# Optimization experiments

Hardware: AMD Instinct MI355X
Metric: run time of the kernel (lower is better)

## Reference

```python
import jax, jax.numpy as jnp
import numpy as np

LOG2 = float(np.log(2.0))
NEG_INF = float('-inf')


def log1mexp(x):
    # numerically accurate log(1 - exp(x)) for x < 0
    return jnp.where(x > -LOG2, jnp.log(-jnp.expm1(x)), jnp.log1p(-jnp.exp(x)))


def encode_input_log(pos):
    neg = log1mexp(pos)
    # interleave [pos_i, neg_i] then prepend constants [-inf (log 0), 0 (log 1)]
    result = jnp.stack([pos, neg], axis=1).reshape(-1)
    constants = jnp.array([NEG_INF, 0.0], dtype=pos.dtype)
    return jnp.concatenate([constants, result])


def sum_layer(x, ptrs, csr, n):
    # product node in log semiring: segment-sum of gathered log-values
    return jax.ops.segment_sum(x[ptrs], csr, num_segments=n)


def logsum_layer(x, ptrs, csr, n, epsilon=1e-15):
    # sum node in log semiring: numerically stable segment log-sum-exp
    g = x[ptrs]
    m = jax.lax.stop_gradient(jax.ops.segment_max(g, csr, num_segments=n))
    z = g - m[csr]
    z = jnp.nan_to_num(z, nan=0.0, posinf=jnp.inf, neginf=-jnp.inf)  # (-inf)-(-inf) -> 0
    s = jax.ops.segment_sum(jnp.exp(z), csr, num_segments=n) + epsilon
    return jnp.log(s) + m


def setup_inputs() -> dict:
    key = jax.random.key(0)
    n_vars = 2_000_000
    deg = 4
    Ns = [4_000_000, 2_000_000, 1_000_000, 500_000]
    sizes_in = [2 + 2 * n_vars] + Ns[:-1]
    ks = jax.random.split(key, 1 + len(Ns))
    # log-probabilities strictly in (log eps, log(1-eps)) so log1mexp is finite
    u = jax.random.uniform(ks[0], (n_vars,), dtype=jnp.float32, minval=1e-6, maxval=1.0 - 1e-6)
    inp = {"weights": jnp.log(u)}
    for i, n in enumerate(Ns):
        e = n * deg
        inp[f"ptrs{i}"] = jax.random.randint(ks[i + 1], (e,), 0, sizes_in[i], dtype=jnp.int32)
        inp[f"csr{i}"] = jnp.repeat(jnp.arange(n, dtype=jnp.int32), deg)  # unrolled CSR, fan-in=deg
        inp[f"n{i}"] = n
    return inp


def reference(weights, ptrs0, csr0, ptrs1, csr1, ptrs2, csr2, ptrs3, csr3, n0, n1, n2, n3):
    x = encode_input_log(weights)
    x = sum_layer(x, ptrs0, csr0, n0)      # layer 0: product (even)
    x = logsum_layer(x, ptrs1, csr1, n1)   # layer 1: sum (odd)
    x = sum_layer(x, ptrs2, csr2, n2)      # layer 2: product
    x = logsum_layer(x, ptrs3, csr3, n3)   # layer 3: sum
    return x
```

## Files before the change

kernel.cpp:

```cpp
#include <hip/hip_runtime.h>
#include <math.h>

#define NEG_INF (-INFINITY)

typedef int      v4i __attribute__((ext_vector_type(4)));
typedef float    v4f __attribute__((ext_vector_type(4)));
typedef _Float16 v4h __attribute__((ext_vector_type(4)));

__device__ __forceinline__ float fast_log1mexp(float v) {
    if (v > -0.125f) {
        float e = v * (1.0f + v * (0.5f + v * (0.16666667f + v * 0.041666667f)));
        return __logf(-e);
    }
    return __logf(1.0f - __expf(v));
}

__global__ __launch_bounds__(256) void cvt_kernel(const float* __restrict__ w,
                                                  _Float16* __restrict__ wh, int n) {
    int i = blockIdx.x * blockDim.x + threadIdx.x;
    int n4 = n >> 2;
    if (i < n4) {
        v4f v = reinterpret_cast<const v4f*>(w)[i];
        v4h o;
        o.x = (_Float16)v.x; o.y = (_Float16)v.y;
        o.z = (_Float16)v.z; o.w = (_Float16)v.w;
        reinterpret_cast<v4h*>(wh)[i] = o;
    }
    int base = n4 << 2;
    if (i < (n - base)) wh[base + i] = (_Float16)w[base + i];
}

__device__ __forceinline__ float decode_h(const _Float16* __restrict__ wh, int p) {
    int j = (p >> 1) - 1;
    float v = (float)wh[j < 0 ? 0 : j];
    float r = (p & 1) ? fast_log1mexp(v) : v;
    if (p < 2) r = (p == 0) ? NEG_INF : 0.0f;
    return r;
}

__global__ __launch_bounds__(256) void sum4_enc_kernel(const _Float16* __restrict__ wh,
                                                       const v4i* __restrict__ ptrs,
                                                       _Float16* __restrict__ y, int n, int h) {
    int t = blockIdx.x * blockDim.x + threadIdx.x;
    if (t >= h) return;
    v4i pA = __builtin_nontemporal_load(ptrs + t);
    int iB = t + h;
    bool hasB = iB < n;
    v4i pB = hasB ? __builtin_nontemporal_load(ptrs + iB) : pA;
    float a = (decode_h(wh, pA.x) + decode_h(wh, pA.y)) + (decode_h(wh, pA.z) + decode_h(wh, pA.w));
    float b = (decode_h(wh, pB.x) + decode_h(wh, pB.y)) + (decode_h(wh, pB.z) + decode_h(wh, pB.w));
    __builtin_nontemporal_store((_Float16)a, y + t);
    if (hasB) __builtin_nontemporal_store((_Float16)b, y + iB);
}

__global__ __launch_bounds__(256) void sum4_h2h_kernel(const _Float16* __restrict__ x,
                                                       const v4i* __restrict__ ptrs,
                                                       _Float16* __restrict__ y, int n, int h) {
    int t = blockIdx.x * blockDim.x + threadIdx.x;
    if (t >= h) return;
    v4i pA = __builtin_nontemporal_load(ptrs + t);
    int iB = t + h;
    bool hasB = iB < n;
    v4i pB = hasB ? __builtin_nontemporal_load(ptrs + iB) : pA;
    float a = ((float)x[pA.x] + (float)x[pA.y]) + ((float)x[pA.z] + (float)x[pA.w]);
    float b = ((float)x[pB.x] + (float)x[pB.y]) + ((float)x[pB.z] + (float)x[pB.w]);
    __builtin_nontemporal_store((_Float16)a, y + t);
    if (hasB) __builtin_nontemporal_store((_Float16)b, y + iB);
}

__device__ __forceinline__ float lse4(float a, float b, float c, float d) {
    float m = fmaxf(fmaxf(a, b), fmaxf(c, d));
    if (m == NEG_INF) return NEG_INF;
    float s = __expf(a - m) + __expf(b - m) + __expf(c - m) + __expf(d - m) + 1e-15f;
    return __logf(s) + m;
}

__global__ __launch_bounds__(256) void logsum4_h2h_kernel(const _Float16* __restrict__ x,
                                                          const v4i* __restrict__ ptrs,
                                                          _Float16* __restrict__ y, int n, int h) {
    int t = blockIdx.x * blockDim.x + threadIdx.x;
    if (t >= h) return;
    v4i pA = __builtin_nontemporal_load(ptrs + t);
    int iB = t + h;
    bool hasB = iB < n;
    v4i pB = hasB ? __builtin_nontemporal_load(ptrs + iB) : pA;
    float a = lse4((float)x[pA.x], (float)x[pA.y], (float)x[pA.z], (float)x[pA.w]);
    float b = lse4((float)x[pB.x], (float)x[pB.y], (float)x[pB.z], (float)x[pB.w]);
    __builtin_nontemporal_store((_Float16)a, y + t);
    if (hasB) __builtin_nontemporal_store((_Float16)b, y + iB);
}

__global__ __launch_bounds__(256) void logsum4_h2f_kernel(const _Float16* __restrict__ x,
                                                          const v4i* __restrict__ ptrs,
                                                          float* __restrict__ y, int n, int h) {
    int t = blockIdx.x * blockDim.x + threadIdx.x;
    if (t >= h) return;
    v4i pA = __builtin_nontemporal_load(ptrs + t);
    int iB = t + h;
    bool hasB = iB < n;
    v4i pB = hasB ? __builtin_nontemporal_load(ptrs + iB) : pA;
    float a = lse4((float)x[pA.x], (float)x[pA.y], (float)x[pA.z], (float)x[pA.w]);
    float b = lse4((float)x[pB.x], (float)x[pB.y], (float)x[pB.z], (float)x[pB.w]);
    __builtin_nontemporal_store(a, y + t);
    if (hasB) __builtin_nontemporal_store(b, y + iB);
}

extern "C" void kernel_launch(void* const* d_in, const int* in_sizes, int n_in,
                              void* d_out, int out_size, void* d_ws, size_t ws_size,
                              hipStream_t stream) {
    const float* w     = (const float*)d_in[0];
    const v4i*   ptrs0 = (const v4i*)d_in[1];
    const v4i*   ptrs1 = (const v4i*)d_in[4];
    const v4i*   ptrs2 = (const v4i*)d_in[7];
    const v4i*   ptrs3 = (const v4i*)d_in[10];

    const int n_vars = in_sizes[0];
    const int n0 = in_sizes[1] / 4;
    const int n1 = in_sizes[4] / 4;
    const int n2 = in_sizes[7] / 4;
    const int n3 = in_sizes[10] / 4;

    char* ws = (char*)d_ws;
    size_t off = 0;
    _Float16* wh = (_Float16*)(ws + off); off += ((size_t)n_vars * 2 + 255) & ~(size_t)255;
    _Float16* y0 = (_Float16*)(ws + off); off += ((size_t)n0 * 2 + 255) & ~(size_t)255;
    _Float16* y1 = (_Float16*)(ws + off); off += ((size_t)n1 * 2 + 255) & ~(size_t)255;
    _Float16* y2 = (_Float16*)(ws + off);
    float* out = (float*)d_out;

    const int B = 256;
    int hc = (n_vars + 3) / 4;
    int h0 = (n0 + 1) / 2, h1 = (n1 + 1) / 2, h2 = (n2 + 1) / 2, h3 = (n3 + 1) / 2;
    cvt_kernel        <<<(hc + B - 1) / B, B, 0, stream>>>(w, wh, n_vars);
    sum4_enc_kernel   <<<(h0 + B - 1) / B, B, 0, stream>>>(wh, ptrs0, y0, n0, h0);
    logsum4_h2h_kernel<<<(h1 + B - 1) / B, B, 0, stream>>>(y0, ptrs1, y1, n1, h1);
    sum4_h2h_kernel   <<<(h2 + B - 1) / B, B, 0, stream>>>(y1, ptrs2, y2, n2, h2);
    logsum4_h2f_kernel<<<(h3 + B - 1) / B, B, 0, stream>>>(y2, ptrs3, out, n3, h3);
}
```

Measured before the change: 376.3 us.

## Split layer-1 gather into two source-half passes and process four outputs per thread

Layer 1 now runs as two passes, each gathering only from one half of the 8 MB fp16 input. The halves are combined with an online log-sum-exp merge through fp32 partial max and sum buffers. This is meant to shrink each pass's random-access working set so it fits better in cache. In exchange, the ptrs array is read twice and the intermediate buffers add about 16 MB of extra traffic. All layers also move from two to four outputs per thread, giving more memory-level parallelism per thread with fewer threads.

```diff
diff --git a/kernel.cpp b/kernel.cpp
--- a/kernel.cpp
+++ b/kernel.cpp
@@ -43,14 +43,14 @@
                                                        _Float16* __restrict__ y, int n, int h) {
     int t = blockIdx.x * blockDim.x + threadIdx.x;
     if (t >= h) return;
-    v4i pA = __builtin_nontemporal_load(ptrs + t);
-    int iB = t + h;
-    bool hasB = iB < n;
-    v4i pB = hasB ? __builtin_nontemporal_load(ptrs + iB) : pA;
-    float a = (decode_h(wh, pA.x) + decode_h(wh, pA.y)) + (decode_h(wh, pA.z) + decode_h(wh, pA.w));
-    float b = (decode_h(wh, pB.x) + decode_h(wh, pB.y)) + (decode_h(wh, pB.z) + decode_h(wh, pB.w));
-    __builtin_nontemporal_store((_Float16)a, y + t);
-    if (hasB) __builtin_nontemporal_store((_Float16)b, y + iB);
+    #pragma unroll
+    for (int k = 0; k < 4; k++) {
+        int i = t + k * h;
+        if (i >= n) break;
+        v4i p = __builtin_nontemporal_load(ptrs + i);
+        float s = (decode_h(wh, p.x) + decode_h(wh, p.y)) + (decode_h(wh, p.z) + decode_h(wh, p.w));
+        __builtin_nontemporal_store((_Float16)s, y + i);
+    }
 }
 
 __global__ __launch_bounds__(256) void sum4_h2h_kernel(const _Float16* __restrict__ x,
@@ -58,14 +58,14 @@
                                                        _Float16* __restrict__ y, int n, int h) {
     int t = blockIdx.x * blockDim.x + threadIdx.x;
     if (t >= h) return;
-    v4i pA = __builtin_nontemporal_load(ptrs + t);
-    int iB = t + h;
-    bool hasB = iB < n;
-    v4i pB = hasB ? __builtin_nontemporal_load(ptrs + iB) : pA;
-    float a = ((float)x[pA.x] + (float)x[pA.y]) + ((float)x[pA.z] + (float)x[pA.w]);
-    float b = ((float)x[pB.x] + (float)x[pB.y]) + ((float)x[pB.z] + (float)x[pB.w]);
-    __builtin_nontemporal_store((_Float16)a, y + t);
-    if (hasB) __builtin_nontemporal_store((_Float16)b, y + iB);
+    #pragma unroll
+    for (int k = 0; k < 4; k++) {
+        int i = t + k * h;
+        if (i >= n) break;
+        v4i p = __builtin_nontemporal_load(ptrs + i);
+        float s = ((float)x[p.x] + (float)x[p.y]) + ((float)x[p.z] + (float)x[p.w]);
+        __builtin_nontemporal_store((_Float16)s, y + i);
+    }
 }
 
 __device__ __forceinline__ float lse4(float a, float b, float c, float d) {
@@ -75,19 +75,62 @@
     return __logf(s) + m;
 }
 
-__global__ __launch_bounds__(256) void logsum4_h2h_kernel(const _Float16* __restrict__ x,
-                                                          const v4i* __restrict__ ptrs,
-                                                          _Float16* __restrict__ y, int n, int h) {
+__global__ __launch_bounds__(256) void l1_passA_kernel(const _Float16* __restrict__ x,
+                                                       const v4i* __restrict__ ptrs,
+                                                       float* __restrict__ mA,
+                                                       float* __restrict__ sA,
+                                                       int n, int h, int half) {
     int t = blockIdx.x * blockDim.x + threadIdx.x;
     if (t >= h) return;
-    v4i pA = __builtin_nontemporal_load(ptrs + t);
-    int iB = t + h;
-    bool hasB = iB < n;
-    v4i pB = hasB ? __builtin_nontemporal_load(ptrs + iB) : pA;
-    float a = lse4((float)x[pA.x], (float)x[pA.y], (float)x[pA.z], (float)x[pA.w]);
-    float b = lse4((float)x[pB.x], (float)x[pB.y], (float)x[pB.z], (float)x[pB.w]);
-    __builtin_nontemporal_store((_Float16)a, y + t);
-    if (hasB) __builtin_nontemporal_store((_Float16)b, y + iB);
+    #pragma unroll
+    for (int k = 0; k < 4; k++) {
+        int i = t + k * h;
+        if (i >= n) break;
+        v4i p = __builtin_nontemporal_load(ptrs + i);
+        float a = (p.x < half) ? (float)x[p.x] : NEG_INF;
+        float b = (p.y < half) ? (float)x[p.y] : NEG_INF;
+        float c = (p.z < half) ? (float)x[p.z] : NEG_INF;
+        float d = (p.w < half) ? (float)x[p.w] : NEG_INF;
+        float m = fmaxf(fmaxf(a, b), fmaxf(c, d));
+        float s = (m == NEG_INF) ? 0.0f
+                : __expf(a - m) + __expf(b - m) + __expf(c - m) + __expf(d - m);
+        __builtin_nontemporal_store(m, mA + i);
+        __builtin_nontemporal_store(s, sA + i);
+    }
+}
+
+__global__ __launch_bounds__(256) void l1_passB_kernel(const _Float16* __restrict__ x,
+                                                       const v4i* __restrict__ ptrs,
+                                                       const float* __restrict__ mA,
+                                                       const float* __restrict__ sA,
+                                                       _Float16* __restrict__ y,
+                                                       int n, int h, int half) {
+    int t = blockIdx.x * blockDim.x + threadIdx.x;
+    if (t >= h) return;
+    #pragma unroll
+    for (int k = 0; k < 4; k++) {
+        int i = t + k * h;
+        if (i >= n) break;
+        v4i p = __builtin_nontemporal_load(ptrs + i);
+        float a = (p.x >= half) ? (float)x[p.x] : NEG_INF;
+        float b = (p.y >= half) ? (float)x[p.y] : NEG_INF;
+        float c = (p.z >= half) ? (float)x[p.z] : NEG_INF;
+        float d = (p.w >= half) ? (float)x[p.w] : NEG_INF;
+        float mB = fmaxf(fmaxf(a, b), fmaxf(c, d));
+        float sB = (mB == NEG_INF) ? 0.0f
+                 : __expf(a - mB) + __expf(b - mB) + __expf(c - mB) + __expf(d - mB);
+        float ma = __builtin_nontemporal_load(mA + i);
+        float sa = __builtin_nontemporal_load(sA + i);
+        float m = fmaxf(ma, mB);
+        float out;
+        if (m == NEG_INF) {
+            out = NEG_INF;
+        } else {
+            float s = sa * __expf(ma - m) + sB * __expf(mB - m) + 1e-15f;
+            out = __logf(s) + m;
+        }
+        __builtin_nontemporal_store((_Float16)out, y + i);
+    }
 }
 
 __global__ __launch_bounds__(256) void logsum4_h2f_kernel(const _Float16* __restrict__ x,
@@ -95,14 +138,14 @@
                                                           float* __restrict__ y, int n, int h) {
     int t = blockIdx.x * blockDim.x + threadIdx.x;
     if (t >= h) return;
-    v4i pA = __builtin_nontemporal_load(ptrs + t);
-    int iB = t + h;
-    bool hasB = iB < n;
-    v4i pB = hasB ? __builtin_nontemporal_load(ptrs + iB) : pA;
-    float a = lse4((float)x[pA.x], (float)x[pA.y], (float)x[pA.z], (float)x[pA.w]);
-    float b = lse4((float)x[pB.x], (float)x[pB.y], (float)x[pB.z], (float)x[pB.w]);
-    __builtin_nontemporal_store(a, y + t);
-    if (hasB) __builtin_nontemporal_store(b, y + iB);
+    #pragma unroll
+    for (int k = 0; k < 4; k++) {
+        int i = t + k * h;
+        if (i >= n) break;
+        v4i p = __builtin_nontemporal_load(ptrs + i);
+        float r = lse4((float)x[p.x], (float)x[p.y], (float)x[p.z], (float)x[p.w]);
+        __builtin_nontemporal_store(r, y + i);
+    }
 }
 
 extern "C" void kernel_launch(void* const* d_in, const int* in_sizes, int n_in,
@@ -125,15 +168,20 @@
     _Float16* wh = (_Float16*)(ws + off); off += ((size_t)n_vars * 2 + 255) & ~(size_t)255;
     _Float16* y0 = (_Float16*)(ws + off); off += ((size_t)n0 * 2 + 255) & ~(size_t)255;
     _Float16* y1 = (_Float16*)(ws + off); off += ((size_t)n1 * 2 + 255) & ~(size_t)255;
-    _Float16* y2 = (_Float16*)(ws + off);
+    _Float16* y2 = (_Float16*)(ws + off); off += ((size_t)n2 * 2 + 255) & ~(size_t)255;
+    float*    mA = (float*)(ws + off);    off += ((size_t)n1 * 4 + 255) & ~(size_t)255;
+    float*    sA = (float*)(ws + off);
     float* out = (float*)d_out;
 
     const int B = 256;
     int hc = (n_vars + 3) / 4;
-    int h0 = (n0 + 1) / 2, h1 = (n1 + 1) / 2, h2 = (n2 + 1) / 2, h3 = (n3 + 1) / 2;
+    int h0 = (n0 + 3) / 4, h1 = (n1 + 3) / 4, h2 = (n2 + 3) / 4, h3 = (n3 + 3) / 4;
+    int half0 = n0 / 2;
+
     cvt_kernel        <<<(hc + B - 1) / B, B, 0, stream>>>(w, wh, n_vars);
     sum4_enc_kernel   <<<(h0 + B - 1) / B, B, 0, stream>>>(wh, ptrs0, y0, n0, h0);
-    logsum4_h2h_kernel<<<(h1 + B - 1) / B, B, 0, stream>>>(y0, ptrs1, y1, n1, h1);
+    l1_passA_kernel   <<<(h1 + B - 1) / B, B, 0, stream>>>(y0, ptrs1, mA, sA, n1, h1, half0);
+    l1_passB_kernel   <<<(h1 + B - 1) / B, B, 0, stream>>>(y0, ptrs1, mA, sA, y1, n1, h1, half0);
     sum4_h2h_kernel   <<<(h2 + B - 1) / B, B, 0, stream>>>(y1, ptrs2, y2, n2, h2);
     logsum4_h2f_kernel<<<(h3 + B - 1) / B, B, 0, stream>>>(y2, ptrs3, out, n3, h3);
 }
```

Measured after the change: 372.1 us. No clear change (-1.1%).
